# Optimization experiments

Measured on AMD Instinct MI355X. Metric: run time of the kernel, lower is better.

## Reference

```python
import jax, jax.numpy as jnp
import numpy as np

N_NODES = 50000
N_EDGES = 800000
MUL0, MUL1 = 16, 8            # multiplicities of 0e and 1o irreps (input == output)
DIM_F = MUL0 + 3 * MUL1       # 40
NRB, NRD = 16, 64             # num_radial_basis, num_radial_dimension
MAX_RADIUS = 5.0
W_NUMEL = MUL0*MUL0 + MUL0*MUL1 + MUL1*MUL1 + MUL1*MUL0  # 576


def _radial_embedding(r):
    # e3nn soft_one_hot_linspace(basis='smooth_finite', cutoff=True), then *sqrt(NRB)
    values = jnp.linspace(0.0, MAX_RADIUS, NRB + 2)[1:-1]
    step = MAX_RADIUS / (NRB + 1)
    d = (r[:, None] - values) / step            # [E, NRB]
    inside = jnp.abs(d) < 1.0
    ds = jnp.where(inside, d, 0.0)              # safe values for the division
    y = 1.14136 * jnp.exp(jnp.float32(2.0)) * jnp.exp(-1.0 / (1.0 + ds)) * jnp.exp(-1.0 / (1.0 - ds))
    return jnp.where(inside, y, 0.0) * jnp.sqrt(jnp.float32(NRB))


def _forward(pos, f_in, W1, W2, edge_src, edge_dst):
    E = edge_src.shape[0]
    N = pos.shape[0]
    # edge geometry
    vec = pos[edge_dst] - pos[edge_src]                       # [E,3]
    r = jnp.sqrt(jnp.sum(vec * vec, axis=1) + 1e-12)          # [E]
    unit = vec / r[:, None]
    sh1 = jnp.sqrt(jnp.float32(3.0)) * unit                   # l=1 SH, component norm; sh0 == 1
    # radial MLP -> per-edge tensor-product weights (e3nn FullyConnectedNet scaling)
    emb = _radial_embedding(r)                                # [E, NRB]
    h = jax.nn.silu(emb @ W1 / jnp.sqrt(jnp.float32(NRB)))    # [E, NRD]
    w = h @ W2 / jnp.sqrt(jnp.float32(NRD))                   # [E, W_NUMEL]
    # gather source node features
    x = f_in[edge_src]                                        # [E, DIM_F]
    x0 = x[:, :MUL0]                                          # [E, 16] scalars (0e)
    x1 = x[:, MUL0:].reshape(E, MUL1, 3)                      # [E, 8, 3] vectors (1o)
    # split per-path 'uvw' weights
    o = MUL0 * MUL0
    w_00 = w[:, :o].reshape(E, MUL0, MUL0)                    # 0e x 0e -> 0e
    w_01 = w[:, o:o + MUL0*MUL1].reshape(E, MUL0, MUL1); o += MUL0*MUL1  # 0e x 1o -> 1o
    w_10 = w[:, o:o + MUL1*MUL1].reshape(E, MUL1, MUL1); o += MUL1*MUL1  # 1o x 0e -> 1o
    w_11 = w[:, o:o + MUL1*MUL0].reshape(E, MUL1, MUL0)                  # 1o x 1o -> 0e
    # path normalization: alpha = sqrt((2*l_out+1)/fan_in); fan_in per output = MUL0 + MUL1
    inv_fan = 1.0 / jnp.sqrt(jnp.float32(MUL0 + MUL1))
    inv_s3 = 1.0 / jnp.sqrt(jnp.float32(3.0))
    # scalar (0e) outputs
    dot = jnp.einsum('euk,ek->eu', x1, sh1)                   # [E, MUL1]
    out0 = inv_fan * (jnp.einsum('euw,eu->ew', w_00, x0)
                      + inv_s3 * jnp.einsum('euw,eu->ew', w_11, dot))
    # vector (1o) outputs
    out1 = inv_fan * (jnp.einsum('euw,eu->ew', w_01, x0)[:, :, None] * sh1[:, None, :]
                      + jnp.einsum('euw,euk->ewk', w_10, x1))
    summand = jnp.concatenate([out0, out1.reshape(E, 3 * MUL1)], axis=1)  # [E, DIM_F]
    f_out = jax.ops.segment_sum(summand, edge_dst, num_segments=N)
    num_neighbors = E / N
    return f_out / jnp.sqrt(jnp.float32(num_neighbors))


def setup_inputs() -> dict:
    key = jax.random.key(0)
    k1, k2, k3, k4, k5, k6 = jax.random.split(key, 6)
    pos = jax.random.normal(k1, (N_NODES, 3), dtype=jnp.float32)
    f_in = jax.random.normal(k2, (N_NODES, DIM_F), dtype=jnp.float32)
    edge_src = jax.random.randint(k3, (N_EDGES,), 0, N_NODES, dtype=jnp.int32)
    edge_dst = jax.random.randint(k4, (N_EDGES,), 0, N_NODES, dtype=jnp.int32)
    W1 = jax.random.normal(k5, (NRB, NRD), dtype=jnp.float32)
    W2 = jax.random.normal(k6, (NRD, W_NUMEL), dtype=jnp.float32)
    return {"pos": pos, "f_in": f_in, "edge_src": edge_src, "edge_dst": edge_dst, "W1": W1, "W2": W2}


def reference(pos, f_in, edge_src, edge_dst, W1, W2):
    return _forward(pos, f_in, W1, W2, edge_src, edge_dst)
```

## Files before the change

kernel.cpp:

```cpp
#include <hip/hip_runtime.h>
#include <hip/hip_fp16.h>

#define N_NODES 50000
#define N_EDGES 800000

typedef short  bf16x8 __attribute__((ext_vector_type(8)));
typedef float  f32x4  __attribute__((ext_vector_type(4)));
typedef _Float16 h16x2 __attribute__((ext_vector_type(2)));

#define FXP32_SCALE 4194304.0f
#define FXP32_INV   2.384185791015625e-07f

#define WSB_BYTES   (36864 * 2)
#define W1P_BYTES   (512 * 4)
#define FB_WORDS    (N_NODES * 20)

__device__ __forceinline__ unsigned short f2bf(float f) {
    unsigned u = __float_as_uint(f);
    u += 0x7FFF + ((u >> 16) & 1);
    return (unsigned short)(u >> 16);
}

__device__ __forceinline__ unsigned pack2bf(float a, float b) {
    return (unsigned)f2bf(a) | ((unsigned)f2bf(b) << 16);
}

__device__ __forceinline__ f32x4 fma4(f32x4 a, f32x4 b, f32x4 c) {
    f32x4 r;
    r[0] = fmaf(a[0], b[0], c[0]);
    r[1] = fmaf(a[1], b[1], c[1]);
    r[2] = fmaf(a[2], b[2], c[2]);
    r[3] = fmaf(a[3], b[3], c[3]);
    return r;
}

#if __has_builtin(__builtin_amdgcn_fdot2)
__device__ __forceinline__ float FDOT2(h16x2 a, h16x2 b, float c) {
    return __builtin_amdgcn_fdot2(a, b, c, false);
}
#else
__device__ __forceinline__ float FDOT2(h16x2 a, h16x2 b, float c) {
    return fmaf((float)a.x, (float)b.x, fmaf((float)a.y, (float)b.y, c));
}
#endif

__global__ void setup_kernel(const float* __restrict__ W2,
                             const float* __restrict__ W1,
                             const float* __restrict__ f_in,
                             unsigned short* __restrict__ wsB,
                             unsigned* __restrict__ w1p,
                             unsigned* __restrict__ fb,
                             int4* __restrict__ out, int n16) {
    int gid = blockIdx.x * 256 + threadIdx.x;
    int nth = gridDim.x * 256;
    for (int i = gid; i < n16; i += nth)
        out[i] = make_int4(0, 0, 0, 0);
    for (int i = gid; i < FB_WORDS; i += nth)
        fb[i] = pack2bf(f_in[2*i], f_in[2*i+1]);
    if (gid < 36864) {
        int j    = gid & 7;
        int lane = (gid >> 3) & 63;
        int ks   = (gid >> 9) & 1;
        int nt   = gid >> 10;
        int k = ks * 32 + (lane >> 4) * 8 + j;
        int n = nt * 16 + (lane & 15);
        wsB[gid] = f2bf(W2[k * 576 + n]);
    } else if (gid < 36864 + 512) {
        int idx = gid - 36864;
        int kk  = idx >> 6;
        int i   = idx & 63;
        __half lo = __float2half(W1[(2*kk)     * 64 + i]);
        __half hi = __float2half(W1[(2*kk + 1) * 64 + i]);
        w1p[idx] = (unsigned)__half_as_ushort(lo)
                 | ((unsigned)__half_as_ushort(hi) << 16);
    }
}

__global__ void finalize_kernel(float4* p, int n4) {
    int i = blockIdx.x * blockDim.x + threadIdx.x;
    if (i < n4) {
        float4 v = p[i];
        float4 f;
        f.x = (float)__float_as_int(v.x) * FXP32_INV;
        f.y = (float)__float_as_int(v.y) * FXP32_INV;
        f.z = (float)__float_as_int(v.z) * FXP32_INV;
        f.w = (float)__float_as_int(v.w) * FXP32_INV;
        p[i] = f;
    }
}

__global__ __launch_bounds__(64, 2) void conv_kernel(
    const float* __restrict__ pos,
    const unsigned* __restrict__ fb,
    const int*   __restrict__ esrc,
    const int*   __restrict__ edst,
    const unsigned* __restrict__ w1p,
    const unsigned short* __restrict__ wsB,
    int*         __restrict__ f_out_i)
{
    __shared__ __align__(16) char smem[9216];

    const int lane = threadIdx.x;
    const int e    = blockIdx.x * 64 + lane;
    char*  my  = smem;
    float* shf = (float*)smem;

    const int s = esrc[e];
    const int d = edst[e];

    const bf16x8* wsBv = (const bf16x8*)wsB;
    bf16x8 bc0 = wsBv[lane],        bc1 = wsBv[64 + lane];
    bf16x8 bn0 = wsBv[128 + lane],  bn1 = wsBv[192 + lane];
    bf16x8 b20, b21;

    float px = pos[3*d+0] - pos[3*s+0];
    float py = pos[3*d+1] - pos[3*s+1];
    float pz = pos[3*d+2] - pos[3*s+2];
    float r  = sqrtf(px*px + py*py + pz*pz + 1e-12f);
    float inv_r = __builtin_amdgcn_rcpf(r);
    float ux = px*inv_r, uy = py*inv_r, uz = pz*inv_r;
    const float SQ3 = 1.7320508075688772f;
    float shx = SQ3*ux, shy = SQ3*uy, shz = SQ3*uz;

    float x0[16], x1[24], dot[8];
    {
        const uint4* xg4 = reinterpret_cast<const uint4*>(fb + (size_t)s * 20);
        uint4 v0 = xg4[0], v1 = xg4[1], v2 = xg4[2], v3 = xg4[3], v4 = xg4[4];
        unsigned xw[20] = {v0.x, v0.y, v0.z, v0.w,
                           v1.x, v1.y, v1.z, v1.w,
                           v2.x, v2.y, v2.z, v2.w,
                           v3.x, v3.y, v3.z, v3.w,
                           v4.x, v4.y, v4.z, v4.w};
        float xr[40];
        #pragma unroll
        for (int i = 0; i < 20; ++i) {
            xr[2*i]   = __uint_as_float(xw[i] << 16);
            xr[2*i+1] = __uint_as_float(xw[i] & 0xffff0000u);
        }
        #pragma unroll
        for (int i = 0; i < 16; ++i) x0[i] = xr[i];
        #pragma unroll
        for (int i = 0; i < 24; ++i) x1[i] = xr[16+i];
        #pragma unroll
        for (int u = 0; u < 8; ++u)
            dot[u] = x1[3*u+0]*ux + x1[3*u+1]*uy + x1[3*u+2]*uz;
    }

    const float A = 1.14136f * 7.38905609893065f;
    const float inv_step = 17.0f / 5.0f;
    float emb[16];
    #pragma unroll
    for (int k = 0; k < 16; ++k) {
        float dd  = r * inv_step - (float)(k + 1);
        float d2v = dd * dd;
        float arg = -2.0f * __builtin_amdgcn_rcpf(1.0f - d2v);
        float val = A * __expf(arg);
        emb[k] = (d2v < 1.0f) ? val : 0.0f;
    }

    unsigned ep[8];
    #pragma unroll
    for (int kk = 0; kk < 8; ++kk) {
        __half lo = __float2half(emb[2*kk]);
        __half hi = __float2half(emb[2*kk+1]);
        ep[kk] = (unsigned)__half_as_ushort(lo)
               | ((unsigned)__half_as_ushort(hi) << 16);
    }
    float h[64];
    #pragma unroll
    for (int i = 0; i < 64; ++i) h[i] = 0.f;
    #pragma unroll
    for (int kk = 0; kk < 8; ++kk) {
        h16x2 ev = __builtin_bit_cast(h16x2, ep[kk]);
        const unsigned* wrow = w1p + kk * 64;
        #pragma unroll
        for (int i = 0; i < 64; ++i) {
            h16x2 wv = __builtin_bit_cast(h16x2, wrow[i]);
            h[i] = FDOT2(ev, wv, h[i]);
        }
    }
    #pragma unroll
    for (int i = 0; i < 64; ++i) {
        float z = h[i];
        h[i] = z * __builtin_amdgcn_rcpf(1.0f + __expf(-z));
    }

    {
        unsigned int hp[32];
        #pragma unroll
        for (int i = 0; i < 32; ++i)
            hp[i] = (unsigned)f2bf(h[2*i]) | ((unsigned)f2bf(h[2*i+1]) << 16);
        uint4* hrow = (uint4*)(my + lane * 144);
        #pragma unroll
        for (int g = 0; g < 8; ++g)
            hrow[g] = make_uint4(hp[4*g], hp[4*g+1], hp[4*g+2], hp[4*g+3]);
    }
    asm volatile("s_waitcnt lgkmcnt(0)" ::: "memory");

    const int q   = lane >> 4;
    const int col = lane & 15;
    const int q4  = q * 4;
    const int ucol = col >> 3;
    bf16x8 aF[4][2];
    #pragma unroll
    for (int mt = 0; mt < 4; ++mt)
        #pragma unroll
        for (int ks = 0; ks < 2; ++ks)
            aF[mt][ks] = *(const bf16x8*)(my + (mt*16 + col)*144 + q*16 + ks*64);
    asm volatile("s_waitcnt lgkmcnt(0)" ::: "memory");

    #pragma unroll
    for (int u = 0; u < 16; ++u) shf[u*64 + lane] = x0[u];
    #pragma unroll
    for (int u = 0; u < 8;  ++u) shf[1024 + u*64 + lane] = dot[u];
    asm volatile("s_waitcnt lgkmcnt(0)" ::: "memory");

    f32x4 out0d[4], t01d[4], o1bd[4][3];
    #pragma unroll
    for (int m = 0; m < 4; ++m) {
        out0d[m] = (f32x4){0.f,0.f,0.f,0.f};
        t01d[m]  = (f32x4){0.f,0.f,0.f,0.f};
        #pragma unroll
        for (int k = 0; k < 3; ++k) o1bd[m][k] = (f32x4){0.f,0.f,0.f,0.f};
    }

#define MFMA8() \
    f32x4 wr0 = {0.f,0.f,0.f,0.f}, wr1 = {0.f,0.f,0.f,0.f}; \
    f32x4 wr2 = {0.f,0.f,0.f,0.f}, wr3 = {0.f,0.f,0.f,0.f}; \
    wr0 = __builtin_amdgcn_mfma_f32_16x16x32_bf16(aF[0][0], bc0, wr0, 0,0,0); \
    wr1 = __builtin_amdgcn_mfma_f32_16x16x32_bf16(aF[1][0], bc0, wr1, 0,0,0); \
    wr2 = __builtin_amdgcn_mfma_f32_16x16x32_bf16(aF[2][0], bc0, wr2, 0,0,0); \
    wr3 = __builtin_amdgcn_mfma_f32_16x16x32_bf16(aF[3][0], bc0, wr3, 0,0,0); \
    wr0 = __builtin_amdgcn_mfma_f32_16x16x32_bf16(aF[0][1], bc1, wr0, 0,0,0); \
    wr1 = __builtin_amdgcn_mfma_f32_16x16x32_bf16(aF[1][1], bc1, wr1, 0,0,0); \
    wr2 = __builtin_amdgcn_mfma_f32_16x16x32_bf16(aF[2][1], bc1, wr2, 0,0,0); \
    wr3 = __builtin_amdgcn_mfma_f32_16x16x32_bf16(aF[3][1], bc1, wr3, 0,0,0);

#define PRE(NT2) { b20 = wsBv[(NT2)*128 + lane]; b21 = wsBv[(NT2)*128 + 64 + lane]; }
#define ROT()    { bc0 = bn0; bc1 = bn1; bn0 = b20; bn1 = b21; }

#define CONS4(ACC, BASEW) { \
    const float* xb_ = shf + (BASEW) + q4; \
    ACC[0] = fma4(wr0, *(const f32x4*)(xb_ +  0), ACC[0]); \
    ACC[1] = fma4(wr1, *(const f32x4*)(xb_ + 16), ACC[1]); \
    ACC[2] = fma4(wr2, *(const f32x4*)(xb_ + 32), ACC[2]); \
    ACC[3] = fma4(wr3, *(const f32x4*)(xb_ + 48), ACC[3]); }

    #pragma unroll
    for (int u = 0; u < 16; ++u) {
        PRE(u + 2);
        MFMA8();
        CONS4(out0d, u * 64);
        ROT();
    }
    #pragma unroll
    for (int t = 0; t < 8; ++t) {
        PRE(t < 6 ? 18 + t : 28 + (t - 6));
        MFMA8();
        CONS4(t01d, (2*t + ucol) * 64);
        ROT();
    }
    #pragma unroll
    for (int m = 0; m < 4; ++m)
        #pragma unroll
        for (int rr = 0; rr < 4; ++rr)
            t01d[m][rr] += __shfl_xor(t01d[m][rr], 8);

    #pragma unroll
    for (int u = 0; u < 8; ++u) {
        PRE(u < 6 ? 30 + u : 24 + (u - 6));
        MFMA8();
        CONS4(out0d, 1024 + u * 64);
        ROT();
    }

    asm volatile("s_waitcnt lgkmcnt(0)" ::: "memory");
    #pragma unroll
    for (int u = 0; u < 8; ++u)
        #pragma unroll
        for (int k = 0; k < 3; ++k)
            shf[(u*3 + k)*64 + lane] = x1[3*u + k];
    asm volatile("s_waitcnt lgkmcnt(0)" ::: "memory");

    #pragma unroll
    for (int t = 0; t < 4; ++t) {
        if (t < 2) PRE(26 + t);
        MFMA8();
        const int ub = (2*t + ucol) * 192 + q4;
#define W10_MT(MT, WR) { \
        f32x4 xv0 = *(const f32x4*)(shf + ub +   0 + 16*(MT)); \
        f32x4 xv1 = *(const f32x4*)(shf + ub +  64 + 16*(MT)); \
        f32x4 xv2 = *(const f32x4*)(shf + ub + 128 + 16*(MT)); \
        o1bd[MT][0] = fma4(WR, xv0, o1bd[MT][0]); \
        o1bd[MT][1] = fma4(WR, xv1, o1bd[MT][1]); \
        o1bd[MT][2] = fma4(WR, xv2, o1bd[MT][2]); }
        W10_MT(0, wr0) W10_MT(1, wr1) W10_MT(2, wr2) W10_MT(3, wr3)
#undef W10_MT
        ROT();
    }
#undef CONS4
#undef PRE
#undef ROT
#undef MFMA8
    #pragma unroll
    for (int m = 0; m < 4; ++m)
        #pragma unroll
        for (int k = 0; k < 3; ++k)
            #pragma unroll
            for (int rr = 0; rr < 4; ++rr)
                o1bd[m][k][rr] += __shfl_xor(o1bd[m][k][rr], 8);

    const float FXP_S = (1.0f / (32.0f * 4.898979485566356f)) * FXP32_SCALE;

    asm volatile("s_waitcnt lgkmcnt(0)" ::: "memory");
    #pragma unroll
    for (int m = 0; m < 4; ++m)
        #pragma unroll
        for (int rr = 0; rr < 4; ++rr)
            shf[(16*m + 4*q + rr) * 20 + col] = out0d[m][rr];
    shf[lane*20 + 16] = shx;
    shf[lane*20 + 17] = shy;
    shf[lane*20 + 18] = shz;
    ((int*)shf)[lane*20 + 19] = d;
    asm volatile("s_waitcnt lgkmcnt(0)" ::: "memory");

    #pragma unroll 4
    for (int it = 0; it < 16; ++it) {
        int p  = it * 64 + lane;
        int ee = p >> 4;
        int c  = p & 15;
        float v = shf[ee*20 + c];
        int dd  = ((int*)shf)[ee*20 + 19];
        atomicAdd(f_out_i + (size_t)dd*40 + c, __float2int_rn(v * FXP_S));
    }

    float shr[4][4][3];
    #pragma unroll
    for (int m = 0; m < 4; ++m)
        #pragma unroll
        for (int rr = 0; rr < 4; ++rr) {
            int eb = (16*m + 4*q + rr) * 20 + 16;
            shr[m][rr][0] = shf[eb + 0];
            shr[m][rr][1] = shf[eb + 1];
            shr[m][rr][2] = shf[eb + 2];
        }
    asm volatile("s_waitcnt lgkmcnt(0)" ::: "memory");
    if (col < 8) {
        #pragma unroll
        for (int m = 0; m < 4; ++m)
            #pragma unroll
            for (int rr = 0; rr < 4; ++rr)
                #pragma unroll
                for (int k = 0; k < 3; ++k) {
                    float fv = fmaf(t01d[m][rr], shr[m][rr][k], o1bd[m][k][rr]);
                    shf[(16*m + 4*q + rr) * 28 + 3*col + k] = fv;
                }
    }
    ((int*)shf)[lane*28 + 27] = d;
    asm volatile("s_waitcnt lgkmcnt(0)" ::: "memory");

    #pragma unroll 4
    for (int it = 0; it < 24; ++it) {
        int p  = it * 64 + lane;
        int ee = (p * 10923) >> 18;
        int c  = p - ee * 24;
        float v = shf[ee*28 + c];
        int dd  = ((int*)shf)[ee*28 + 27];
        atomicAdd(f_out_i + (size_t)dd*40 + 16 + c, __float2int_rn(v * FXP_S));
    }
}

extern "C" void kernel_launch(void* const* d_in, const int* in_sizes, int n_in,
                              void* d_out, int out_size, void* d_ws, size_t ws_size,
                              hipStream_t stream) {
    const float* pos  = (const float*)d_in[0];
    const float* f_in = (const float*)d_in[1];
    const int*   esrc = (const int*)  d_in[2];
    const int*   edst = (const int*)  d_in[3];
    const float* W1   = (const float*)d_in[4];
    const float* W2   = (const float*)d_in[5];
    float* out = (float*)d_out;

    unsigned short* wsB = (unsigned short*)d_ws;
    unsigned*       w1p = (unsigned*)((char*)d_ws + WSB_BYTES);
    unsigned*       fb  = (unsigned*)((char*)d_ws + WSB_BYTES + W1P_BYTES);

    const int nOut = N_NODES * 40;
    const int n16  = nOut / 4;

    setup_kernel<<<512, 256, 0, stream>>>(W2, W1, f_in, wsB, w1p, fb,
                                          (int4*)out, n16);

    conv_kernel<<<N_EDGES / 64, 64, 0, stream>>>(
        pos, fb, esrc, edst, w1p, wsB, (int*)out);

    finalize_kernel<<<(n16 + 255) / 256, 256, 0, stream>>>((float4*)out, n16);
}
```

Baseline: 230.0 us.

## Fuse finalize pass into conv kernel via last-blocks completion counter

Removes the separate finalize kernel launch. Each conv block increments a global done counter, and the last FIN_BLOCKS blocks spin-wait until all tiles have finished, then convert the fixed-point accumulators to float in place. This saves one kernel launch and its boundary, at the cost of an extra atomic per block and spinning blocks that hold CU slots near the tail. Correctness relies on the waiting blocks being resident while earlier blocks are still scheduled.

```diff
diff --git a/kernel.cpp b/kernel.cpp
--- a/kernel.cpp
+++ b/kernel.cpp
@@ -3,6 +3,8 @@
 
 #define N_NODES 50000
 #define N_EDGES 800000
+#define N_TILES (N_EDGES / 64)
+#define FIN_BLOCKS 512
 
 typedef short  bf16x8 __attribute__((ext_vector_type(8)));
 typedef float  f32x4  __attribute__((ext_vector_type(4)));
@@ -14,6 +16,7 @@
 #define WSB_BYTES   (36864 * 2)
 #define W1P_BYTES   (512 * 4)
 #define FB_WORDS    (N_NODES * 20)
+#define DONE_OFF    (WSB_BYTES + W1P_BYTES + FB_WORDS * 4)
 
 __device__ __forceinline__ unsigned short f2bf(float f) {
     unsigned u = __float_as_uint(f);
@@ -50,9 +53,11 @@
                              unsigned short* __restrict__ wsB,
                              unsigned* __restrict__ w1p,
                              unsigned* __restrict__ fb,
+                             unsigned* __restrict__ done_ctr,
                              int4* __restrict__ out, int n16) {
     int gid = blockIdx.x * 256 + threadIdx.x;
     int nth = gridDim.x * 256;
+    if (gid == 0) *done_ctr = 0u;
     for (int i = gid; i < n16; i += nth)
         out[i] = make_int4(0, 0, 0, 0);
     for (int i = gid; i < FB_WORDS; i += nth)
@@ -76,19 +81,6 @@
     }
 }
 
-__global__ void finalize_kernel(float4* p, int n4) {
-    int i = blockIdx.x * blockDim.x + threadIdx.x;
-    if (i < n4) {
-        float4 v = p[i];
-        float4 f;
-        f.x = (float)__float_as_int(v.x) * FXP32_INV;
-        f.y = (float)__float_as_int(v.y) * FXP32_INV;
-        f.z = (float)__float_as_int(v.z) * FXP32_INV;
-        f.w = (float)__float_as_int(v.w) * FXP32_INV;
-        p[i] = f;
-    }
-}
-
 __global__ __launch_bounds__(64, 2) void conv_kernel(
     const float* __restrict__ pos,
     const unsigned* __restrict__ fb,
@@ -96,6 +88,7 @@
     const int*   __restrict__ edst,
     const unsigned* __restrict__ w1p,
     const unsigned short* __restrict__ wsB,
+    unsigned*    __restrict__ done_ctr,
     int*         __restrict__ f_out_i)
 {
     __shared__ __align__(16) char smem[9216];
@@ -368,6 +361,30 @@
         int dd  = ((int*)shf)[ee*28 + 27];
         atomicAdd(f_out_i + (size_t)dd*40 + 16 + c, __float2int_rn(v * FXP_S));
     }
+
+    __threadfence();
+    unsigned t = 0;
+    if (lane == 0) t = atomicAdd(done_ctr, 1u);
+    t = __shfl(t, 0);
+    if (t >= (unsigned)(N_TILES - FIN_BLOCKS)) {
+        if (lane == 0) {
+            while (atomicAdd(done_ctr, 0u) < (unsigned)N_TILES)
+                __builtin_amdgcn_s_sleep(4);
+        }
+        __threadfence();
+        const int slot = (int)t - (N_TILES - FIN_BLOCKS);
+        float4* p4 = (float4*)f_out_i;
+        const int n16 = (N_NODES * 40) / 4;
+        for (int i = slot * 64 + lane; i < n16; i += FIN_BLOCKS * 64) {
+            float4 v = p4[i];
+            float4 f;
+            f.x = (float)__float_as_int(v.x) * FXP32_INV;
+            f.y = (float)__float_as_int(v.y) * FXP32_INV;
+            f.z = (float)__float_as_int(v.z) * FXP32_INV;
+            f.w = (float)__float_as_int(v.w) * FXP32_INV;
+            p4[i] = f;
+        }
+    }
 }
 
 extern "C" void kernel_launch(void* const* d_in, const int* in_sizes, int n_in,
@@ -381,18 +398,17 @@
     const float* W2   = (const float*)d_in[5];
     float* out = (float*)d_out;
 
-    unsigned short* wsB = (unsigned short*)d_ws;
-    unsigned*       w1p = (unsigned*)((char*)d_ws + WSB_BYTES);
-    unsigned*       fb  = (unsigned*)((char*)d_ws + WSB_BYTES + W1P_BYTES);
+    unsigned short* wsB  = (unsigned short*)d_ws;
+    unsigned*       w1p  = (unsigned*)((char*)d_ws + WSB_BYTES);
+    unsigned*       fb   = (unsigned*)((char*)d_ws + WSB_BYTES + W1P_BYTES);
+    unsigned*       done = (unsigned*)((char*)d_ws + DONE_OFF);
 
     const int nOut = N_NODES * 40;
     const int n16  = nOut / 4;
 
-    setup_kernel<<<512, 256, 0, stream>>>(W2, W1, f_in, wsB, w1p, fb,
+    setup_kernel<<<512, 256, 0, stream>>>(W2, W1, f_in, wsB, w1p, fb, done,
                                           (int4*)out, n16);
 
-    conv_kernel<<<N_EDGES / 64, 64, 0, stream>>>(
-        pos, fb, esrc, edst, w1p, wsB, (int*)out);
-
-    finalize_kernel<<<(n16 + 255) / 256, 256, 0, stream>>>((float4*)out, n16);
-}
+    conv_kernel<<<N_TILES, 64, 0, stream>>>(
+        pos, fb, esrc, edst, w1p, wsB, done, (int*)out);
+}
```

Result: slower. 553.4 us (+140.6%).
